# Kernel tuning notes

Measured on AMD Instinct MI355X. Metric: run time of the kernel, lower is better.

## Reference

```python
import jax, jax.numpy as jnp
import numpy as np

B, N = 32, 262144

def setup_inputs() -> dict:
    key = jax.random.key(0)
    k1, k2, k3, k4, k5 = jax.random.split(key, 5)
    F_mat = jax.random.normal(k1, (B, 3, 3), jnp.float32)
    f = 800.0 + 50.0 * jax.random.normal(k2, (B,), jnp.float32)
    K = (jnp.zeros((B, 3, 3), jnp.float32)
         .at[:, 0, 0].set(f).at[:, 1, 1].set(f)
         .at[:, 0, 2].set(320.0).at[:, 1, 2].set(240.0)
         .at[:, 2, 2].set(1.0))
    pts1_flat = jax.random.uniform(k3, (N, 2), jnp.float32) * 640.0
    pts2_flat = jax.random.uniform(k4, (N, 2), jnp.float32) * 640.0
    batch_indices = jnp.sort(jax.random.randint(k5, (N,), 0, B))
    return {"F_mat": F_mat, "K": K, "pts1_flat": pts1_flat,
            "pts2_flat": pts2_flat, "batch_indices": batch_indices}

def _pose_candidates(E):
    # torch.svd returns V (not V^T); the original code uses R = U @ W @ V.
    U, S, Vh = jnp.linalg.svd(E)
    U = U * jnp.where(jnp.linalg.det(U) < 0, -1.0, 1.0)[:, None, None]
    Vh = Vh * jnp.where(jnp.linalg.det(Vh) < 0, -1.0, 1.0)[:, None, None]
    V = jnp.swapaxes(Vh, -1, -2)  # = torch's "Vt" variable (which is V)
    W = jnp.array([[0.0, -1.0, 0.0], [1.0, 0.0, 0.0], [0.0, 0.0, 1.0]], E.dtype)
    R1 = U @ W @ V
    R2 = U @ W.T @ V
    t = U[:, :, 2]
    R_cand = jnp.stack([R1, R1, R2, R2], axis=1)          # [B,4,3,3]
    t_cand = jnp.stack([t, -t, t, -t], axis=1)            # [B,4,3]
    return R_cand, t_cand

def _cheirality_scores(R_cand, t_cand, K, pts1_flat, pts2_flat, batch_indices):
    n = pts1_flat.shape[0]
    Kinv = jnp.linalg.inv(K)[batch_indices]               # [N,3,3]
    ones = jnp.ones((n, 1), pts1_flat.dtype)
    p1 = jnp.einsum('nij,nj->ni', Kinv, jnp.concatenate([pts1_flat, ones], 1))[:, :2]
    p2 = jnp.einsum('nij,nj->ni', Kinv, jnp.concatenate([pts2_flat, ones], 1))[:, :2]
    P2 = jnp.concatenate([R_cand, t_cand[..., None]], axis=-1)  # [B,4,3,4]
    P2n = P2[batch_indices]                                     # [N,4,3,4]
    # A rows for P1 = [I|0]: A0 = [-1,0,x1,0], A1 = [0,-1,y1,0]
    z = jnp.zeros((n,), p1.dtype)
    A0 = jnp.stack([-jnp.ones_like(z), z, p1[:, 0], z], axis=-1)  # [N,4]
    A1 = jnp.stack([z, -jnp.ones_like(z), p1[:, 1], z], axis=-1)
    A2 = p2[:, 0, None, None] * P2n[:, :, 2, :] - P2n[:, :, 0, :]  # [N,4,4]
    A3 = p2[:, 1, None, None] * P2n[:, :, 2, :] - P2n[:, :, 1, :]
    A = jnp.stack([jnp.broadcast_to(A0[:, None, :], A2.shape),
                   jnp.broadcast_to(A1[:, None, :], A2.shape), A2, A3], axis=2)  # [N,4,4,4]
    _, _, Vh = jnp.linalg.svd(A)
    vec = Vh[..., :, -1]                      # = last ROW of V, faithful to torch code
    pts3d = vec[..., :3] / vec[..., 3:4]      # [N,4,3]
    z1 = pts3d[..., 2]                        # depth in cam 1 (P1 = [I|0])
    z2 = jnp.sum(P2n[:, :, 2, :3] * pts3d, axis=-1) + P2n[:, :, 2, 3]
    in_front = ((z1 > 0) & (z2 > 0)).astype(jnp.float32)  # [N,4]
    scores = jax.ops.segment_sum(in_front, batch_indices, num_segments=B)  # [B,4]
    counts = jax.ops.segment_sum(jnp.ones((n,), jnp.float32), batch_indices, num_segments=B)
    return scores, counts

def reference(F_mat, K, pts1_flat, pts2_flat, batch_indices):
    E = jnp.einsum('bji,bjk,bkl->bil', K, F_mat, K)       # K^T F K
    R_cand, t_cand = _pose_candidates(E)
    scores, counts = _cheirality_scores(R_cand, t_cand, K, pts1_flat, pts2_flat, batch_indices)
    best_idx = jnp.argmax(scores, axis=1)                 # first max, like torch '>'
    has = (counts > 0).astype(R_cand.dtype)
    bi = jnp.arange(B)
    best_R = R_cand[bi, best_idx] * has[:, None, None]
    best_t = t_cand[bi, best_idx] * has[:, None]
    best_candidate = jnp.where(counts > 0, best_idx, 0)
    return best_R, best_t, best_candidate
```

## Files before the change

### kernel.cpp

```cpp
#include <hip/hip_runtime.h>
#include <math.h>


#define NBATCH 32
#define USE_NEW_SLARTG 1

#define EPS4  5.9604645e-08f
#define UNFL4 1.1754944e-38f
#define TOL4  (10.0f * EPS4)


__device__ __forceinline__ float sign_f(float a, float b) {
  return (b >= 0.0f) ? fabsf(a) : -fabsf(a);
}

__device__ __forceinline__ float slapy2f(float x, float y) {
#pragma clang fp contract(off)
  float xa = fabsf(x), ya = fabsf(y);
  float w = fmaxf(xa, ya), z = fminf(xa, ya);
  if (z == 0.0f) return w;
  float r = z / w;
  return w * sqrtf(1.0f + r * r);
}

// ... 89 lines not shown
      float mm_ = gt / ft;
      float t = 2.0f - l;
      float mm = mm_ * mm_, tt = t * t;
      float s = sqrtf(tt + mm);
      float r;
      if (l == 0.0f) r = fabsf(mm_); else r = sqrtf(l * l + mm);
      float a = 0.5f * (s + r);
      *ssmin = ha / a;
      *ssmax = fa * a;
      if (mm == 0.0f) {
        if (l == 0.0f) t = sign_f(2.0f, ft) * sign_f(1.0f, gt);
        else t = gt / sign_f(dd, ft) + mm_ / t;
      } else {
        t = (mm_ / (s + t) + mm_ / (r + l)) * (1.0f + a);
      }
      float l2 = sqrtf(t * t + 4.0f);
      crt = 2.0f / l2;
      srt = t / l2;
      clt = (crt + srt * mm_) / a;
      slt = (ht / ft) * srt / a;
    }
  }
  if (swap_) { *csl = srt; *snl = crt; *csr = slt; *snr = clt; }
  else { *csl = clt; *snl = slt; *csr = crt; *snr = srt; }
  float tsign = 1.0f;
  if (pmax == 1) tsign = sign_f(1.0f, *csr) * sign_f(1.0f, *csl) * sign_f(1.0f, f);
  if (pmax == 2) tsign = sign_f(1.0f, *snr) * sign_f(1.0f, *csl) * sign_f(1.0f, g);
  if (pmax == 3) tsign = sign_f(1.0f, *snr) * sign_f(1.0f, *snl) * sign_f(1.0f, h);
  *ssmax = sign_f(*ssmax, tsign);
  *ssmin = sign_f(*ssmin, tsign * sign_f(1.0f, f) * sign_f(1.0f, h));
}


template <int NN, bool WANTU>
__device__ void sbdsqr_t(float* d, float* e, float VT[4][4], float U[4][4]) {
#pragma clang fp contract(off)
  const int n = NN;
  const float EPS = EPS4;
  const float UNFL = UNFL4;
  const float TOL = TOL4;
  const int MAXITR = 6;

  float sminoa = fabsf(d[0]);
  if (sminoa != 0.0f) {
    float mu = sminoa;
    for (int i = 2; i <= n; i++) {
      mu = fabsf(d[i - 1]) * (mu / (mu + fabsf(e[i - 2])));
      if (mu < sminoa) sminoa = mu;
      if (sminoa == 0.0f) break;
    }
  }
  sminoa = sminoa / sqrtf((float)n);
  float thresh = fmaxf(TOL * sminoa, (float)(MAXITR * n * n) * UNFL);

  int maxit = MAXITR * n * n;
  int iter = 0, oldll = -1, oldm = -1, idir = 0;
  int m = n;
  float sminl = 0.0f;
  int guard = 0;

  while (guard++ < 1000) {
    if (m <= 1) break;
    if (iter > maxit) break;

    float smax = fabsf(d[m - 1]);
    float smin = smax; (void)smin;
    int ll = 0;
    bool split = false;
    for (int lll = 1; lll <= m - 1; lll++) {
      ll = m - lll;
      float abss = fabsf(d[ll - 1]);
      float abse = fabsf(e[ll - 1]);
      if (abse <= thresh) { split = true; break; }
      if (abss < smin) smin = abss;
      float mx = fmaxf(abss, abse);
      if (mx > smax) smax = mx;
    }
    if (split) {
      e[ll - 1] = 0.0f;
      if (ll == m - 1) { m = m - 1; continue; }
      ll = ll + 1;
    } else {
      ll = 1;
    }
    if (ll == m - 1) {
      float sigmn, sigmx, sinr, cosr, sinl, cosl;
      slasv2_(d[m - 2], e[m - 2], d[m - 1], &sigmn, &sigmx, &sinr, &cosr, &sinl, &cosl);
      d[m - 2] = sigmx; e[m - 2] = 0.0f; d[m - 1] = sigmn;
      for (int k = 0; k < n; k++) {
        float x = VT[m - 2][k], y = VT[m - 1][k];
        VT[m - 2][k] = cosr * x + sinr * y; VT[m - 1][k] = cosr * y - sinr * x;
      }
      if (WANTU) {
        for (int k = 0; k < n; k++) {
          float x = U[k][m - 2], y = U[k][m - 1];
          U[k][m - 2] = cosl * x + sinl * y; U[k][m - 1] = cosl * y - sinl * x;
        }
      }
      m -= 2;
      continue;
    }
    if (ll > oldm || m < oldll)
      idir = (fabsf(d[ll - 1]) >= fabsf(d[m - 1])) ? 1 : 2;

    bool deflated = false;
    if (idir == 1) {
      if (fabsf(e[m - 2]) <= TOL * fabsf(d[m - 1])) { e[m - 2] = 0.0f; continue; }
      float mu = fabsf(d[ll - 1]); sminl = mu;
      for (int lll = ll; lll <= m - 1; lll++) {
        if (fabsf(e[lll - 1]) <= TOL * mu) { e[lll - 1] = 0.0f; deflated = true; break; }
        mu = fabsf(d[lll]) * (mu / (mu + fabsf(e[lll - 1])));
        if (mu < sminl) sminl = mu;
      }
    } else {
      if (fabsf(e[ll - 1]) <= TOL * fabsf(d[ll - 1])) { e[ll - 1] = 0.0f; continue; }
      float mu = fabsf(d[m - 1]); sminl = mu;
      for (int lll = m - 1; lll >= ll; lll--) {
        if (fabsf(e[lll - 1]) <= TOL * mu) { e[lll - 1] = 0.0f; deflated = true; break; }
        mu = fabsf(d[lll - 1]) * (mu / (mu + fabsf(e[lll - 1])));
        if (mu < sminl) sminl = mu;
      }
    }
    if (deflated) continue;
    oldll = ll; oldm = m;

    float shift = 0.0f, rdum;
    if (!((float)n * TOL * (sminl / smax) <= fmaxf(EPS, 0.01f * TOL))) {
      float sll;
      if (idir == 1) { sll = fabsf(d[ll - 1]); slas2_(d[m - 2], e[m - 2], d[m - 1], &shift, &rdum); }
      else { sll = fabsf(d[m - 1]); slas2_(d[ll - 1], e[ll - 1], d[ll], &shift, &rdum); }
      if (sll > 0.0f) {
        float q = shift / sll;
        if (q * q < EPS) shift = 0.0f;
      }
    }
    iter += m - ll;

    if (shift == 0.0f) {
      if (idir == 1) {
        float cs = 1.0f, oldcs = 1.0f, sn = 0.0f, oldsn = 0.0f, r = 0.0f;
        for (int i = ll; i <= m - 1; i++) {
          float c1, s1;
          slartg_(d[i - 1] * cs, e[i - 1], &c1, &s1, &r);
          cs = c1; sn = s1;
          if (i > ll) e[i - 2] = oldsn * r;
          float c2, s2, rr;
          slartg_(oldcs * r, d[i] * sn, &c2, &s2, &rr);
          oldcs = c2; oldsn = s2;
          d[i - 1] = rr;
          for (int k = 0; k < n; k++) {
            float x = VT[i - 1][k], y = VT[i][k];
            VT[i - 1][k] = cs * x + sn * y; VT[i][k] = cs * y - sn * x;
          }
          if (WANTU) {
            for (int k = 0; k < n; k++) {
              float x = U[k][i - 1], y = U[k][i];
              U[k][i - 1] = oldcs * x + oldsn * y; U[k][i] = oldcs * y - oldsn * x;
            }
          }
        }
        float h = d[m - 1] * cs;
        d[m - 1] = h * oldcs;
        e[m - 2] = h * oldsn;
        if (fabsf(e[m - 2]) <= thresh) e[m - 2] = 0.0f;
      } else {
        float cs = 1.0f, oldcs = 1.0f, sn = 0.0f, oldsn = 0.0f, r = 0.0f;
        for (int i = m; i >= ll + 1; i--) {
          float c1, s1;
          slartg_(d[i - 1] * cs, e[i - 2], &c1, &s1, &r);
          cs = c1; sn = s1;
          if (i < m) e[i - 1] = oldsn * r;
          float c2, s2, rr;
          slartg_(oldcs * r, d[i - 2] * sn, &c2, &s2, &rr);
          oldcs = c2; oldsn = s2;
          d[i - 1] = rr;
          if (WANTU) {
            for (int k = 0; k < n; k++) {
              float x = U[k][i - 1], y = U[k][i - 2];
              U[k][i - 1] = cs * x + sn * y; U[k][i - 2] = cs * y - sn * x;
            }
          }
          for (int k = 0; k < n; k++) {
            float x = VT[i - 1][k], y = VT[i - 2][k];
            VT[i - 1][k] = oldcs * x + oldsn * y; VT[i - 2][k] = oldcs * y - oldsn * x;
          }
        }
        float h = d[ll - 1] * cs;
        d[ll - 1] = h * oldcs;
        e[ll - 1] = h * oldsn;
        if (fabsf(e[ll - 1]) <= thresh) e[ll - 1] = 0.0f;
      }
    } else {
      if (idir == 1) {
        float f = (fabsf(d[ll - 1]) - shift) * (sign_f(1.0f, d[ll - 1]) + shift / d[ll - 1]);
        float g = e[ll - 1];
        for (int i = ll; i <= m - 1; i++) {
          float cosr, sinr, r;
          slartg_(f, g, &cosr, &sinr, &r);
          if (i > ll) e[i - 2] = r;
          f = cosr * d[i - 1] + sinr * e[i - 1];
          e[i - 1] = cosr * e[i - 1] - sinr * d[i - 1];
          g = sinr * d[i];
          d[i] = cosr * d[i];
          float cosl, sinl, rr;
          slartg_(f, g, &cosl, &sinl, &rr);
          d[i - 1] = rr;
          f = cosl * e[i - 1] + sinl * d[i];
          d[i] = cosl * d[i] - sinl * e[i - 1];
          if (i < m - 1) {
            g = sinl * e[i];
            e[i] = cosl * e[i];
          }
          for (int k = 0; k < n; k++) {
            float x = VT[i - 1][k], y = VT[i][k];
            VT[i - 1][k] = cosr * x + sinr * y; VT[i][k] = cosr * y - sinr * x;
          }
          if (WANTU) {
            for (int k = 0; k < n; k++) {
              float x = U[k][i - 1], y = U[k][i];
              U[k][i - 1] = cosl * x + sinl * y; U[k][i] = cosl * y - sinl * x;
            }
          }
        }
        e[m - 2] = f;
        if (fabsf(e[m - 2]) <= thresh) e[m - 2] = 0.0f;
      } else {
        float f = (fabsf(d[m - 1]) - shift) * (sign_f(1.0f, d[m - 1]) + shift / d[m - 1]);
        float g = e[m - 2];
        for (int i = m; i >= ll + 1; i--) {
          float cosr, sinr, r;
          slartg_(f, g, &cosr, &sinr, &r);
          if (i < m) e[i - 1] = r;
          f = cosr * d[i - 1] + sinr * e[i - 2];
          e[i - 2] = cosr * e[i - 2] - sinr * d[i - 1];
          g = sinr * d[i - 2];
          d[i - 2] = cosr * d[i - 2];
          float cosl, sinl, rr;
          slartg_(f, g, &cosl, &sinl, &rr);
          d[i - 1] = rr;
          f = cosl * e[i - 2] + sinl * d[i - 2];
          d[i - 2] = cosl * d[i - 2] - sinl * e[i - 2];
          if (i > ll + 1) {
            g = sinl * e[i - 3];
            e[i - 3] = cosl * e[i - 3];
          }
          if (WANTU) {
            for (int k = 0; k < n; k++) {
              float x = U[k][i - 1], y = U[k][i - 2];
              U[k][i - 1] = cosr * x + sinr * y; U[k][i - 2] = cosr * y - sinr * x;
            }
          }
          for (int k = 0; k < n; k++) {
            float x = VT[i - 1][k], y = VT[i - 2][k];
            VT[i - 1][k] = cosl * x + sinl * y; VT[i - 2][k] = cosl * y - sinl * x;
          }
        }
        e[ll - 1] = f;
        if (fabsf(e[ll - 1]) <= thresh) e[ll - 1] = 0.0f;
      }
    }
  }

  for (int i = 0; i < n; i++) {
    if (d[i] < 0.0f) {
      d[i] = -d[i];
      for (int k = 0; k < n; k++) VT[i][k] = -VT[i][k];
    }
  }
  for (int i = 1; i <= n - 1; i++) {
    int isub = 1; float smn = d[0];
    for (int j = 2; j <= n + 1 - i; j++) {
      if (d[j - 1] <= smn) { isub = j; smn = d[j - 1]; }
    }
    if (isub != n + 1 - i) {
      d[isub - 1] = d[n - i]; d[n - i] = smn;
      for (int k = 0; k < n; k++) { float t = VT[isub - 1][k]; VT[isub - 1][k] = VT[n - i][k]; VT[n - i][k] = t; }
      if (WANTU) {
        for (int k = 0; k < n; k++) { float t = U[k][isub - 1]; U[k][isub - 1] = U[k][n - i]; U[k][n - i] = t; }
      }
    }
  }
}

template <int NN, bool WANTU>
__device__ void gesdd_small(const float* A0, float U[4][4], float VT[4][4]) {
#pragma clang fp contract(off)
  const int n = NN;
  float a[4][4];
  for (int i = 0; i < n; i++) for (int j = 0; j < n; j++) a[i][j] = A0[i * n + j];
  float d[4], e[4], tauq[4], taup[4];

  for (int i = 0; i < n; i++) {
    float alpha = a[i][i];
    float ss = 0.0f;
    for (int r = i + 1; r < n; r++) ss += a[r][i] * a[r][i];
    if (ss == 0.0f) { tauq[i] = 0.0f; d[i] = alpha; }
    else {
      float xnorm = sqrtf(ss);
      float beta = -sign_f(slapy2f(alpha, xnorm), alpha);
      tauq[i] = (beta - alpha) / beta;
      float scal = 1.0f / (alpha - beta);
      for (int r = i + 1; r < n; r++) a[r][i] *= scal;
      d[i] = beta;
    }
    for (int c = i + 1; c < n; c++) {
      float w = a[i][c];
      for (int r = i + 1; r < n; r++) w += a[r][i] * a[r][c];
      float tw = tauq[i] * w;
      a[i][c] -= tw;
      for (int r = i + 1; r < n; r++) a[r][c] -= tw * a[r][i];
    }
    if (i < n - 1) {
      float alpha2 = a[i][i + 1];
      float ss2 = 0.0f;
      for (int c = i + 2; c < n; c++) ss2 += a[i][c] * a[i][c];
      if (ss2 == 0.0f) { taup[i] = 0.0f; e[i] = alpha2; }
      else {
        float xnorm = sqrtf(ss2);
        float beta = -sign_f(slapy2f(alpha2, xnorm), alpha2);
        taup[i] = (beta - alpha2) / beta;
        float scal = 1.0f / (alpha2 - beta);
        for (int c = i + 2; c < n; c++) a[i][c] *= scal;
        e[i] = beta;
      }
      for (int r = i + 1; r < n; r++) {
        float w = a[r][i + 1];
        for (int c = i + 2; c < n; c++) w += a[r][c] * a[i][c];
        float tw = taup[i] * w;
        a[r][i + 1] -= tw;
        for (int c = i + 2; c < n; c++) a[r][c] -= tw * a[i][c];
      }
    }
  }

  for (int i = 0; i < n; i++) for (int j = 0; j < n; j++) {
    VT[i][j] = (i == j) ? 1.0f : 0.0f;
    if (WANTU) U[i][j] = (i == j) ? 1.0f : 0.0f;
  }
  sbdsqr_t<NN, WANTU>(d, e, VT, U);

  if (WANTU) {
    for (int i = n - 1; i >= 0; i--) {
      for (int c = 0; c < n; c++) {
        float w = U[i][c];
        for (int r = i + 1; r < n; r++) w += a[r][i] * U[r][c];
        float tw = tauq[i] * w;
        U[i][c] -= tw;
        for (int r = i + 1; r < n; r++) U[r][c] -= tw * a[r][i];
      }
    }
  }
  for (int i = n - 2; i >= 0; i--) {
    for (int r = 0; r < n; r++) {
      float w = VT[r][i + 1];
      for (int c = i + 2; c < n; c++) w += VT[r][c] * a[i][c];
      float tw = taup[i] * w;
      VT[r][i + 1] -= tw;
      for (int c = i + 2; c < n; c++) VT[r][c] -= tw * a[i][c];
    }
  }
}

__device__ __forceinline__ float det3f(const float M[4][4]) {
#pragma clang fp contract(off)
  return M[0][0] * (M[1][1] * M[2][2] - M[1][2] * M[2][1])
       - M[0][1] * (M[1][0] * M[2][2] - M[1][2] * M[2][0])
       + M[0][2] * (M[1][0] * M[2][1] - M[1][1] * M[2][0]);
}


template <int LL, int M>
__device__ __forceinline__ void sv_chase(float (&d)[4], float (&e)[3], float (&vt)[4][4],
                                         float thresh, int& iter, int& oldll, int& oldm,
                                         int& idir, float smax) {
#pragma clang fp contract(off)
  if (LL > oldm || M < oldll)
    idir = (fabsf(d[LL - 1]) >= fabsf(d[M - 1])) ? 1 : 2;

  bool deflated = false;
  float sminl = 0.0f;
  if (idir == 1) {
    if (fabsf(e[M - 2]) <= TOL4 * fabsf(d[M - 1])) { e[M - 2] = 0.0f; return; }
    float mu = fabsf(d[LL - 1]); sminl = mu;
#pragma unroll
    for (int lll = LL; lll <= M - 1; lll++) {
      if (!deflated) {
        if (fabsf(e[lll - 1]) <= TOL4 * mu) { e[lll - 1] = 0.0f; deflated = true; }
        else {
          mu = fabsf(d[lll]) * (mu / (mu + fabsf(e[lll - 1])));
          if (mu < sminl) sminl = mu;
        }
      }
    }
  } else {
    if (fabsf(e[LL - 1]) <= TOL4 * fabsf(d[LL - 1])) { e[LL - 1] = 0.0f; return; }
    float mu = fabsf(d[M - 1]); sminl = mu;
// ... 361 lines not shown
    vt[r][1] -= tw;
    vt[r][2] -= tw * a[0][2];
    vt[r][3] -= tw * a[0][3];
  }

  vec[0] = vt[0][3]; vec[1] = vt[1][3]; vec[2] = vt[2][3]; vec[3] = vt[3][3];
}


__global__ __launch_bounds__(64) void pose_kernel(const float* __restrict__ Fm,
                                                  const float* __restrict__ Km,
                                                  float* __restrict__ ws) {
  int b = blockIdx.x;
  if (threadIdx.x != 0 || b >= NBATCH) return;
  float* wsR = ws;
  float* wsT = ws + 1152;
  float* wsK = ws + 1536;
  int* scores = (int*)(ws + 1664);
  int* counts = (int*)(ws + 1792);
  for (int c = 0; c < 4; c++) scores[b * 4 + c] = 0;
  counts[b] = 0;
  {
#pragma clang fp contract(off)
    const float* F = Fm + b * 9;
    const float* K = Km + b * 9;
    float E[9];
    for (int i = 0; i < 3; i++) for (int l = 0; l < 3; l++) {
      float acc = 0.0f;
      for (int j = 0; j < 3; j++)
        for (int k = 0; k < 3; k++)
          acc += (K[j * 3 + i] * F[j * 3 + k]) * K[k * 3 + l];
      E[i * 3 + l] = acc;
    }
    float U[4][4], VT[4][4];
    gesdd_small<3, true>(E, U, VT);
    float su = (det3f(U) < 0.0f) ? -1.0f : 1.0f;
    float sv = (det3f(VT) < 0.0f) ? -1.0f : 1.0f;
    for (int i = 0; i < 3; i++) for (int j = 0; j < 3; j++) { U[i][j] *= su; VT[i][j] *= sv; }
    float R1[3][3], R2[3][3];
    for (int r = 0; r < 3; r++) {
      float uw0 = U[r][1], uw1 = -U[r][0], uw2 = U[r][2];
      float vw0 = -U[r][1], vw1 = U[r][0];
      for (int c = 0; c < 3; c++) {
        R1[r][c] = (uw0 * VT[c][0] + uw1 * VT[c][1]) + uw2 * VT[c][2];
        R2[r][c] = (vw0 * VT[c][0] + vw1 * VT[c][1]) + uw2 * VT[c][2];
      }
    }
    float t0 = U[0][2], t1 = U[1][2], t2 = U[2][2];
    for (int c = 0; c < 4; c++) {
      const float (*R)[3] = (c < 2) ? R1 : R2;
      float sg = (c & 1) ? -1.0f : 1.0f;
      float* dst = wsR + (b * 4 + c) * 9;
      for (int i = 0; i < 3; i++) for (int j = 0; j < 3; j++) dst[i * 3 + j] = R[i][j];
      float* dt = wsT + (b * 4 + c) * 3;
      dt[0] = sg * t0; dt[1] = sg * t1; dt[2] = sg * t2;
    }
    const float fx = K[0], fy = K[4], cx = K[2], cy = K[5];
    float invfx = 1.0f / fx, invfy = 1.0f / fy;
    wsK[b * 4 + 0] = invfx;
    wsK[b * 4 + 1] = -(invfx * cx);
    wsK[b * 4 + 2] = invfy;
    wsK[b * 4 + 3] = -(invfy * cy);
  }
}


__global__ __launch_bounds__(256) void score_kernel(const float* __restrict__ pts1,
                                                    const float* __restrict__ pts2,
                                                    const int* __restrict__ bidx,
                                                    float* __restrict__ ws,
                                                    int n_pts) {
  __shared__ float sR[1152];
  __shared__ float sT[384];
  __shared__ float sK[128];
  __shared__ int h01[32], h23[32], hc[32];
  int tid = threadIdx.x;
  for (int i = tid; i < 1152; i += 256) sR[i] = ws[i];
  for (int i = tid; i < 384; i += 256) sT[i] = ws[1152 + i];
  for (int i = tid; i < 128; i += 256) sK[i] = ws[1536 + i];
  if (tid < 32) { h01[tid] = 0; h23[tid] = 0; hc[tid] = 0; }
  __syncthreads();

  int gid = blockIdx.x * 256 + tid;
  int n = gid >> 1, pr = gid & 1;
  bool active = (n < n_pts);
  bool f0 = false, f1 = false;
  int b = 0;
  if (active) {
    b = bidx[n];
    float x1 = pts1[2 * n], y1 = pts1[2 * n + 1];
    float x2 = pts2[2 * n], y2 = pts2[2 * n + 1];
    float invfx = sK[b * 4 + 0], k02 = sK[b * 4 + 1];
    float invfy = sK[b * 4 + 2], k12 = sK[b * 4 + 3];
    const float* R = sR + (b * 4 + 2 * pr) * 9;
    const float* t = sT + (b * 4 + 2 * pr) * 3;
    float Am[16];
    float row2[4] = { R[6], R[7], R[8], t[2] };
    {
#pragma clang fp contract(off)
      float p1x = invfx * x1 + k02;
      float p1y = invfy * y1 + k12;
      float p2x = invfx * x2 + k02;
      float p2y = invfy * y2 + k12;
      float row0[4] = { R[0], R[1], R[2], t[0] };
      float row1[4] = { R[3], R[4], R[5], t[1] };
      Am[0] = -1.0f; Am[1] = 0.0f; Am[2] = p1x; Am[3] = 0.0f;
      Am[4] = 0.0f; Am[5] = -1.0f; Am[6] = p1y; Am[7] = 0.0f;
#pragma unroll
      for (int k = 0; k < 4; k++) {
        Am[8 + k] = p2x * row2[k] - row0[k];
        Am[12 + k] = p2y * row2[k] - row1[k];
      }
    }
    float vec[4];
    gesdd4_vec(Am, vec);
    {
#pragma clang fp contract(off)
      float v3 = vec[3];
      float X = vec[0] / v3, Y = vec[1] / v3, Z = vec[2] / v3;
      float p0 = row2[0] * X, p1 = row2[1] * Y, p2 = row2[2] * Z;
      float s = (p0 + p1) + p2;
      float t2 = row2[3];
      float z2a = s + t2;
      float z2b = s + (-t2);
      bool zpos = (Z > 0.0f);
      f0 = zpos && (z2a > 0.0f);
      f1 = zpos && (z2b > 0.0f);
    }
  }
  if (active) {
    int add = (f0 ? 1 : 0) | (f1 ? (1 << 16) : 0);
    if (add) {
      if (pr == 0) atomicAdd(&h01[b], add);
      else atomicAdd(&h23[b], add);
    }
    if (pr == 0) atomicAdd(&hc[b], 1);
  }
  __syncthreads();
  if (tid < 32) {
    int* scores = (int*)(ws + 1664);
    int* counts = (int*)(ws + 1792);
    int v01 = h01[tid], v23 = h23[tid], vc = hc[tid];
    if (v01 & 0xFFFF) atomicAdd(&scores[tid * 4 + 0], v01 & 0xFFFF);
    if (v01 >> 16) atomicAdd(&scores[tid * 4 + 1], v01 >> 16);
    if (v23 & 0xFFFF) atomicAdd(&scores[tid * 4 + 2], v23 & 0xFFFF);
    if (v23 >> 16) atomicAdd(&scores[tid * 4 + 3], v23 >> 16);
    if (vc) atomicAdd(&counts[tid], vc);
  }
}


__global__ __launch_bounds__(64) void final_kernel(const float* __restrict__ ws,
                                                   float* __restrict__ out) {
  int b = threadIdx.x;
  if (b >= NBATCH) return;
  const int* scores = (const int*)(ws + 1664);
  const int* counts = (const int*)(ws + 1792);
  int best = 0, bs = scores[b * 4];
  for (int c = 1; c < 4; c++) {
    int sc = scores[b * 4 + c];
    if (sc > bs) { bs = sc; best = c; }
  }
  int cnt = counts[b];
  float has = (cnt > 0) ? 1.0f : 0.0f;
  const float* R = ws + (b * 4 + best) * 9;
  const float* t = ws + 1152 + (b * 4 + best) * 3;
  for (int k = 0; k < 9; k++) out[b * 9 + k] = R[k] * has;
  for (int k = 0; k < 3; k++) out[288 + b * 3 + k] = t[k] * has;
  out[384 + b] = (cnt > 0) ? (float)best : 0.0f;
}


extern "C" void kernel_launch(void* const* d_in, const int* in_sizes, int n_in,
                              void* d_out, int out_size, void* d_ws, size_t ws_size,
                              hipStream_t stream) {
  (void)n_in; (void)out_size; (void)ws_size;
  const float* F = (const float*)d_in[0];
  const float* K = (const float*)d_in[1];
  const float* p1 = (const float*)d_in[2];
  const float* p2 = (const float*)d_in[3];
  const int* bi = (const int*)d_in[4];
  int n_pts = in_sizes[4];
  float* ws = (float*)d_ws;
  float* out = (float*)d_out;

  pose_kernel<<<NBATCH, 64, 0, stream>>>(F, K, ws);
  int total = n_pts * 2;
  int blocks = (total + 255) / 256;
  score_kernel<<<blocks, 256, 0, stream>>>(p1, p2, bi, ws, n_pts);
  final_kernel<<<1, 64, 0, stream>>>(ws, out);
}
```

Before: 219.8 us.

## Specialize pose SVD to 3x3, drop shared staging, use wave-ballot score reduction

Replaces the generic templated bidiagonal SVD in the pose kernel with a fully unrolled 3x3-specialized version. In the score kernel it removes shared-memory staging of R, t and K in favour of direct global reads, and halves the block size to 128. It also replaces the shared-memory histogram and per-block flush with wave-level ballot/popcount reductions that issue global atomics directly, falling back to per-thread atomics when a wave spans several batches. The aim is to cut per-block setup and barriers in the dominant score kernel. In exchange, more global atomics reach the same addresses.

```diff
diff --git a/kernel.cpp b/kernel.cpp
--- a/kernel.cpp
+++ b/kernel.cpp
@@ -145,336 +145,462 @@
 }
 
 
-template <int NN, bool WANTU>
-__device__ void sbdsqr_t(float* d, float* e, float VT[4][4], float U[4][4]) {
-#pragma clang fp contract(off)
-  const int n = NN;
-  const float EPS = EPS4;
-  const float UNFL = UNFL4;
-  const float TOL = TOL4;
-  const int MAXITR = 6;
-
-  float sminoa = fabsf(d[0]);
-  if (sminoa != 0.0f) {
-    float mu = sminoa;
-    for (int i = 2; i <= n; i++) {
-      mu = fabsf(d[i - 1]) * (mu / (mu + fabsf(e[i - 2])));
-      if (mu < sminoa) sminoa = mu;
-      if (sminoa == 0.0f) break;
-    }
-  }
-  sminoa = sminoa / sqrtf((float)n);
-  float thresh = fmaxf(TOL * sminoa, (float)(MAXITR * n * n) * UNFL);
-
-  int maxit = MAXITR * n * n;
-  int iter = 0, oldll = -1, oldm = -1, idir = 0;
-  int m = n;
+__device__ __forceinline__ void sv3_chase(float (&d)[3], float (&e)[2],
+                                          float (&vt)[3][3], float (&u)[3][3],
+                                          float thresh, int& iter, int& oldll,
+                                          int& oldm, int& idir, float smax) {
+#pragma clang fp contract(off)
+  if (1 > oldm || 3 < oldll)
+    idir = (fabsf(d[0]) >= fabsf(d[2])) ? 1 : 2;
+
+  bool deflated = false;
   float sminl = 0.0f;
-  int guard = 0;
-
-  while (guard++ < 1000) {
-    if (m <= 1) break;
-    if (iter > maxit) break;
-
-    float smax = fabsf(d[m - 1]);
-    float smin = smax; (void)smin;
-    int ll = 0;
-    bool split = false;
-    for (int lll = 1; lll <= m - 1; lll++) {
-      ll = m - lll;
-      float abss = fabsf(d[ll - 1]);
-      float abse = fabsf(e[ll - 1]);
-      if (abse <= thresh) { split = true; break; }
-      if (abss < smin) smin = abss;
-      float mx = fmaxf(abss, abse);
-      if (mx > smax) smax = mx;
-    }
-    if (split) {
-      e[ll - 1] = 0.0f;
-      if (ll == m - 1) { m = m - 1; continue; }
-      ll = ll + 1;
+  if (idir == 1) {
+    if (fabsf(e[1]) <= TOL4 * fabsf(d[2])) { e[1] = 0.0f; return; }
+    float mu = fabsf(d[0]); sminl = mu;
+    if (fabsf(e[0]) <= TOL4 * mu) { e[0] = 0.0f; deflated = true; }
+    else {
+      mu = fabsf(d[1]) * (mu / (mu + fabsf(e[0])));
+      if (mu < sminl) sminl = mu;
+      if (fabsf(e[1]) <= TOL4 * mu) { e[1] = 0.0f; deflated = true; }
+      else {
+        mu = fabsf(d[2]) * (mu / (mu + fabsf(e[1])));
+        if (mu < sminl) sminl = mu;
+      }
+    }
+  } else {
+    if (fabsf(e[0]) <= TOL4 * fabsf(d[0])) { e[0] = 0.0f; return; }
+    float mu = fabsf(d[2]); sminl = mu;
+    if (fabsf(e[1]) <= TOL4 * mu) { e[1] = 0.0f; deflated = true; }
+    else {
+      mu = fabsf(d[1]) * (mu / (mu + fabsf(e[1])));
+      if (mu < sminl) sminl = mu;
+      if (fabsf(e[0]) <= TOL4 * mu) { e[0] = 0.0f; deflated = true; }
+      else {
+        mu = fabsf(d[0]) * (mu / (mu + fabsf(e[0])));
+        if (mu < sminl) sminl = mu;
+      }
+    }
+  }
+  if (deflated) return;
+  oldll = 1; oldm = 3;
+
+  float shift = 0.0f, rdum;
+  if (!(3.0f * TOL4 * (sminl / smax) <= fmaxf(EPS4, 0.01f * TOL4))) {
+    float sll;
+    if (idir == 1) { sll = fabsf(d[0]); slas2_(d[1], e[1], d[2], &shift, &rdum); }
+    else { sll = fabsf(d[2]); slas2_(d[0], e[0], d[1], &shift, &rdum); }
+    if (sll > 0.0f) {
+      float q = shift / sll;
+      if (q * q < EPS4) shift = 0.0f;
+    }
+  }
+  iter += 2;
+
+  if (shift == 0.0f) {
+    if (idir == 1) {
+      float cs = 1.0f, oldcs = 1.0f, sn = 0.0f, oldsn = 0.0f, r = 0.0f;
+      float c1, s1, c2, s2, rr;
+      slartg_(d[0] * cs, e[0], &c1, &s1, &r); cs = c1; sn = s1;
+      slartg_(oldcs * r, d[1] * sn, &c2, &s2, &rr); oldcs = c2; oldsn = s2;
+      d[0] = rr;
+#pragma unroll
+      for (int k = 0; k < 3; k++) {
+        float x = vt[0][k], y = vt[1][k];
+        vt[0][k] = cs * x + sn * y; vt[1][k] = cs * y - sn * x;
+      }
+#pragma unroll
+      for (int k = 0; k < 3; k++) {
+        float x = u[k][0], y = u[k][1];
+        u[k][0] = oldcs * x + oldsn * y; u[k][1] = oldcs * y - oldsn * x;
+      }
+      slartg_(d[1] * cs, e[1], &c1, &s1, &r); cs = c1; sn = s1;
+      e[0] = oldsn * r;
+      slartg_(oldcs * r, d[2] * sn, &c2, &s2, &rr); oldcs = c2; oldsn = s2;
+      d[1] = rr;
+#pragma unroll
+      for (int k = 0; k < 3; k++) {
+        float x = vt[1][k], y = vt[2][k];
+        vt[1][k] = cs * x + sn * y; vt[2][k] = cs * y - sn * x;
+      }
+#pragma unroll
+      for (int k = 0; k < 3; k++) {
+        float x = u[k][1], y = u[k][2];
+        u[k][1] = oldcs * x + oldsn * y; u[k][2] = oldcs * y - oldsn * x;
+      }
+      float h = d[2] * cs;
+      d[2] = h * oldcs;
+      e[1] = h * oldsn;
+      if (fabsf(e[1]) <= thresh) e[1] = 0.0f;
     } else {
+      float cs = 1.0f, oldcs = 1.0f, sn = 0.0f, oldsn = 0.0f, r = 0.0f;
+      float c1, s1, c2, s2, rr;
+      slartg_(d[2] * cs, e[1], &c1, &s1, &r); cs = c1; sn = s1;
+      slartg_(oldcs * r, d[1] * sn, &c2, &s2, &rr); oldcs = c2; oldsn = s2;
+      d[2] = rr;
+#pragma unroll
+      for (int k = 0; k < 3; k++) {
+        float x = u[k][2], y = u[k][1];
+        u[k][2] = cs * x + sn * y; u[k][1] = cs * y - sn * x;
+      }
+#pragma unroll
+      for (int k = 0; k < 3; k++) {
+        float x = vt[2][k], y = vt[1][k];
+        vt[2][k] = oldcs * x + oldsn * y; vt[1][k] = oldcs * y - oldsn * x;
+      }
+      slartg_(d[1] * cs, e[0], &c1, &s1, &r); cs = c1; sn = s1;
+      e[1] = oldsn * r;
+      slartg_(oldcs * r, d[0] * sn, &c2, &s2, &rr); oldcs = c2; oldsn = s2;
+      d[1] = rr;
+#pragma unroll
+      for (int k = 0; k < 3; k++) {
+        float x = u[k][1], y = u[k][0];
+        u[k][1] = cs * x + sn * y; u[k][0] = cs * y - sn * x;
+      }
+#pragma unroll
+      for (int k = 0; k < 3; k++) {
+        float x = vt[1][k], y = vt[0][k];
+        vt[1][k] = oldcs * x + oldsn * y; vt[0][k] = oldcs * y - oldsn * x;
+      }
+      float h = d[0] * cs;
+      d[0] = h * oldcs;
+      e[0] = h * oldsn;
+      if (fabsf(e[0]) <= thresh) e[0] = 0.0f;
+    }
+  } else {
+    if (idir == 1) {
+      float f = (fabsf(d[0]) - shift) * (sign_f(1.0f, d[0]) + shift / d[0]);
+      float g = e[0];
+      float cosr, sinr, cosl, sinl, r, rr;
+      slartg_(f, g, &cosr, &sinr, &r);
+      f = cosr * d[0] + sinr * e[0];
+      e[0] = cosr * e[0] - sinr * d[0];
+      g = sinr * d[1];
+      d[1] = cosr * d[1];
+      slartg_(f, g, &cosl, &sinl, &rr);
+      d[0] = rr;
+      f = cosl * e[0] + sinl * d[1];
+      d[1] = cosl * d[1] - sinl * e[0];
+      g = sinl * e[1];
+      e[1] = cosl * e[1];
+#pragma unroll
+      for (int k = 0; k < 3; k++) {
+        float x = vt[0][k], y = vt[1][k];
+        vt[0][k] = cosr * x + sinr * y; vt[1][k] = cosr * y - sinr * x;
+      }
+#pragma unroll
+      for (int k = 0; k < 3; k++) {
+        float x = u[k][0], y = u[k][1];
+        u[k][0] = cosl * x + sinl * y; u[k][1] = cosl * y - sinl * x;
+      }
+      slartg_(f, g, &cosr, &sinr, &r);
+      e[0] = r;
+      f = cosr * d[1] + sinr * e[1];
+      e[1] = cosr * e[1] - sinr * d[1];
+      g = sinr * d[2];
+      d[2] = cosr * d[2];
+      slartg_(f, g, &cosl, &sinl, &rr);
+      d[1] = rr;
+      f = cosl * e[1] + sinl * d[2];
+      d[2] = cosl * d[2] - sinl * e[1];
+#pragma unroll
+      for (int k = 0; k < 3; k++) {
+        float x = vt[1][k], y = vt[2][k];
+        vt[1][k] = cosr * x + sinr * y; vt[2][k] = cosr * y - sinr * x;
+      }
+#pragma unroll
+      for (int k = 0; k < 3; k++) {
+        float x = u[k][1], y = u[k][2];
+        u[k][1] = cosl * x + sinl * y; u[k][2] = cosl * y - sinl * x;
+      }
+      e[1] = f;
+      if (fabsf(e[1]) <= thresh) e[1] = 0.0f;
+    } else {
+      float f = (fabsf(d[2]) - shift) * (sign_f(1.0f, d[2]) + shift / d[2]);
+      float g = e[1];
+      float cosr, sinr, cosl, sinl, r, rr;
+      slartg_(f, g, &cosr, &sinr, &r);
+      f = cosr * d[2] + sinr * e[1];
+      e[1] = cosr * e[1] - sinr * d[2];
+      g = sinr * d[1];
+      d[1] = cosr * d[1];
+      slartg_(f, g, &cosl, &sinl, &rr);
+      d[2] = rr;
+      f = cosl * e[1] + sinl * d[1];
+      d[1] = cosl * d[1] - sinl * e[1];
+      g = sinl * e[0];
+      e[0] = cosl * e[0];
+#pragma unroll
+      for (int k = 0; k < 3; k++) {
+        float x = u[k][2], y = u[k][1];
+        u[k][2] = cosr * x + sinr * y; u[k][1] = cosr * y - sinr * x;
+      }
+#pragma unroll
+      for (int k = 0; k < 3; k++) {
+        float x = vt[2][k], y = vt[1][k];
+        vt[2][k] = cosl * x + sinl * y; vt[1][k] = cosl * y - sinl * x;
+      }
+      slartg_(f, g, &cosr, &sinr, &r);
+      e[1] = r;
+      f = cosr * d[1] + sinr * e[0];
+      e[0] = cosr * e[0] - sinr * d[1];
+      g = sinr * d[0];
+      d[0] = cosr * d[0];
+      slartg_(f, g, &cosl, &sinl, &rr);
+      d[1] = rr;
+      f = cosl * e[0] + sinl * d[0];
+      d[0] = cosl * d[0] - sinl * e[0];
+#pragma unroll
+      for (int k = 0; k < 3; k++) {
+        float x = u[k][1], y = u[k][0];
+        u[k][1] = cosr * x + sinr * y; u[k][0] = cosr * y - sinr * x;
+      }
+#pragma unroll
+      for (int k = 0; k < 3; k++) {
+        float x = vt[1][k], y = vt[0][k];
+        vt[1][k] = cosl * x + sinl * y; vt[0][k] = cosl * y - sinl * x;
+      }
+      e[0] = f;
+      if (fabsf(e[0]) <= thresh) e[0] = 0.0f;
+    }
+  }
+}
+
+__device__ __forceinline__ void sv3_iter3(float (&d)[3], float (&e)[2],
+                                          float (&vt)[3][3], float (&u)[3][3],
+                                          float thresh, int& m, int& iter,
+                                          int& oldll, int& oldm, int& idir) {
+#pragma clang fp contract(off)
+  float smax = fabsf(d[2]);
+  int ll = 0;
+  bool split = false;
+  if (fabsf(e[1]) <= thresh) { split = true; ll = 2; }
+  else {
+    smax = fmaxf(smax, fmaxf(fabsf(d[1]), fabsf(e[1])));
+    if (fabsf(e[0]) <= thresh) { split = true; ll = 1; }
+    else {
+      smax = fmaxf(smax, fmaxf(fabsf(d[0]), fabsf(e[0])));
       ll = 1;
     }
-    if (ll == m - 1) {
-      float sigmn, sigmx, sinr, cosr, sinl, cosl;
-      slasv2_(d[m - 2], e[m - 2], d[m - 1], &sigmn, &sigmx, &sinr, &cosr, &sinl, &cosl);
-      d[m - 2] = sigmx; e[m - 2] = 0.0f; d[m - 1] = sigmn;
-      for (int k = 0; k < n; k++) {
-        float x = VT[m - 2][k], y = VT[m - 1][k];
-        VT[m - 2][k] = cosr * x + sinr * y; VT[m - 1][k] = cosr * y - sinr * x;
-      }
-      if (WANTU) {
-        for (int k = 0; k < n; k++) {
-          float x = U[k][m - 2], y = U[k][m - 1];
-          U[k][m - 2] = cosl * x + sinl * y; U[k][m - 1] = cosl * y - sinl * x;
-        }
-      }
-      m -= 2;
-      continue;
-    }
-    if (ll > oldm || m < oldll)
-      idir = (fabsf(d[ll - 1]) >= fabsf(d[m - 1])) ? 1 : 2;
-
-    bool deflated = false;
-    if (idir == 1) {
-      if (fabsf(e[m - 2]) <= TOL * fabsf(d[m - 1])) { e[m - 2] = 0.0f; continue; }
-      float mu = fabsf(d[ll - 1]); sminl = mu;
-      for (int lll = ll; lll <= m - 1; lll++) {
-        if (fabsf(e[lll - 1]) <= TOL * mu) { e[lll - 1] = 0.0f; deflated = true; break; }
-        mu = fabsf(d[lll]) * (mu / (mu + fabsf(e[lll - 1])));
-        if (mu < sminl) sminl = mu;
-      }
-    } else {
-      if (fabsf(e[ll - 1]) <= TOL * fabsf(d[ll - 1])) { e[ll - 1] = 0.0f; continue; }
-      float mu = fabsf(d[m - 1]); sminl = mu;
-      for (int lll = m - 1; lll >= ll; lll--) {
-        if (fabsf(e[lll - 1]) <= TOL * mu) { e[lll - 1] = 0.0f; deflated = true; break; }
-        mu = fabsf(d[lll - 1]) * (mu / (mu + fabsf(e[lll - 1])));
-        if (mu < sminl) sminl = mu;
-      }
-    }
-    if (deflated) continue;
-    oldll = ll; oldm = m;
-
-    float shift = 0.0f, rdum;
-    if (!((float)n * TOL * (sminl / smax) <= fmaxf(EPS, 0.01f * TOL))) {
-      float sll;
-      if (idir == 1) { sll = fabsf(d[ll - 1]); slas2_(d[m - 2], e[m - 2], d[m - 1], &shift, &rdum); }
-      else { sll = fabsf(d[m - 1]); slas2_(d[ll - 1], e[ll - 1], d[ll], &shift, &rdum); }
-      if (sll > 0.0f) {
-        float q = shift / sll;
-        if (q * q < EPS) shift = 0.0f;
-      }
-    }
-    iter += m - ll;
-
-    if (shift == 0.0f) {
-      if (idir == 1) {
-        float cs = 1.0f, oldcs = 1.0f, sn = 0.0f, oldsn = 0.0f, r = 0.0f;
-        for (int i = ll; i <= m - 1; i++) {
-          float c1, s1;
-          slartg_(d[i - 1] * cs, e[i - 1], &c1, &s1, &r);
-          cs = c1; sn = s1;
-          if (i > ll) e[i - 2] = oldsn * r;
-          float c2, s2, rr;
-          slartg_(oldcs * r, d[i] * sn, &c2, &s2, &rr);
-          oldcs = c2; oldsn = s2;
-          d[i - 1] = rr;
-          for (int k = 0; k < n; k++) {
-            float x = VT[i - 1][k], y = VT[i][k];
-            VT[i - 1][k] = cs * x + sn * y; VT[i][k] = cs * y - sn * x;
-          }
-          if (WANTU) {
-            for (int k = 0; k < n; k++) {
-              float x = U[k][i - 1], y = U[k][i];
-              U[k][i - 1] = oldcs * x + oldsn * y; U[k][i] = oldcs * y - oldsn * x;
-            }
-          }
-        }
-        float h = d[m - 1] * cs;
-        d[m - 1] = h * oldcs;
-        e[m - 2] = h * oldsn;
-        if (fabsf(e[m - 2]) <= thresh) e[m - 2] = 0.0f;
-      } else {
-        float cs = 1.0f, oldcs = 1.0f, sn = 0.0f, oldsn = 0.0f, r = 0.0f;
-        for (int i = m; i >= ll + 1; i--) {
-          float c1, s1;
-          slartg_(d[i - 1] * cs, e[i - 2], &c1, &s1, &r);
-          cs = c1; sn = s1;
-          if (i < m) e[i - 1] = oldsn * r;
-          float c2, s2, rr;
-          slartg_(oldcs * r, d[i - 2] * sn, &c2, &s2, &rr);
-          oldcs = c2; oldsn = s2;
-          d[i - 1] = rr;
-          if (WANTU) {
-            for (int k = 0; k < n; k++) {
-              float x = U[k][i - 1], y = U[k][i - 2];
-              U[k][i - 1] = cs * x + sn * y; U[k][i - 2] = cs * y - sn * x;
-            }
-          }
-          for (int k = 0; k < n; k++) {
-            float x = VT[i - 1][k], y = VT[i - 2][k];
-            VT[i - 1][k] = oldcs * x + oldsn * y; VT[i - 2][k] = oldcs * y - oldsn * x;
-          }
-        }
-        float h = d[ll - 1] * cs;
-        d[ll - 1] = h * oldcs;
-        e[ll - 1] = h * oldsn;
-        if (fabsf(e[ll - 1]) <= thresh) e[ll - 1] = 0.0f;
-      }
-    } else {
-      if (idir == 1) {
-        float f = (fabsf(d[ll - 1]) - shift) * (sign_f(1.0f, d[ll - 1]) + shift / d[ll - 1]);
-        float g = e[ll - 1];
-        for (int i = ll; i <= m - 1; i++) {
-          float cosr, sinr, r;
-          slartg_(f, g, &cosr, &sinr, &r);
-          if (i > ll) e[i - 2] = r;
-          f = cosr * d[i - 1] + sinr * e[i - 1];
-          e[i - 1] = cosr * e[i - 1] - sinr * d[i - 1];
-          g = sinr * d[i];
-          d[i] = cosr * d[i];
-          float cosl, sinl, rr;
-          slartg_(f, g, &cosl, &sinl, &rr);
-          d[i - 1] = rr;
-          f = cosl * e[i - 1] + sinl * d[i];
-          d[i] = cosl * d[i] - sinl * e[i - 1];
-          if (i < m - 1) {
-            g = sinl * e[i];
-            e[i] = cosl * e[i];
-          }
-          for (int k = 0; k < n; k++) {
-            float x = VT[i - 1][k], y = VT[i][k];
-            VT[i - 1][k] = cosr * x + sinr * y; VT[i][k] = cosr * y - sinr * x;
-          }
-          if (WANTU) {
-            for (int k = 0; k < n; k++) {
-              float x = U[k][i - 1], y = U[k][i];
-              U[k][i - 1] = cosl * x + sinl * y; U[k][i] = cosl * y - sinl * x;
-            }
-          }
-        }
-        e[m - 2] = f;
-        if (fabsf(e[m - 2]) <= thresh) e[m - 2] = 0.0f;
-      } else {
-        float f = (fabsf(d[m - 1]) - shift) * (sign_f(1.0f, d[m - 1]) + shift / d[m - 1]);
-        float g = e[m - 2];
-        for (int i = m; i >= ll + 1; i--) {
-          float cosr, sinr, r;
-          slartg_(f, g, &cosr, &sinr, &r);
-          if (i < m) e[i - 1] = r;
-          f = cosr * d[i - 1] + sinr * e[i - 2];
-          e[i - 2] = cosr * e[i - 2] - sinr * d[i - 1];
-          g = sinr * d[i - 2];
-          d[i - 2] = cosr * d[i - 2];
-          float cosl, sinl, rr;
-          slartg_(f, g, &cosl, &sinl, &rr);
-          d[i - 1] = rr;
-          f = cosl * e[i - 2] + sinl * d[i - 2];
-          d[i - 2] = cosl * d[i - 2] - sinl * e[i - 2];
-          if (i > ll + 1) {
-            g = sinl * e[i - 3];
-            e[i - 3] = cosl * e[i - 3];
-          }
-          if (WANTU) {
-            for (int k = 0; k < n; k++) {
-              float x = U[k][i - 1], y = U[k][i - 2];
-              U[k][i - 1] = cosr * x + sinr * y; U[k][i - 2] = cosr * y - sinr * x;
-            }
-          }
-          for (int k = 0; k < n; k++) {
-            float x = VT[i - 1][k], y = VT[i - 2][k];
-            VT[i - 1][k] = cosl * x + sinl * y; VT[i - 2][k] = cosl * y - sinl * x;
-          }
-        }
-        e[ll - 1] = f;
-        if (fabsf(e[ll - 1]) <= thresh) e[ll - 1] = 0.0f;
-      }
-    }
-  }
-
-  for (int i = 0; i < n; i++) {
-    if (d[i] < 0.0f) {
-      d[i] = -d[i];
-      for (int k = 0; k < n; k++) VT[i][k] = -VT[i][k];
-    }
-  }
-  for (int i = 1; i <= n - 1; i++) {
-    int isub = 1; float smn = d[0];
-    for (int j = 2; j <= n + 1 - i; j++) {
-      if (d[j - 1] <= smn) { isub = j; smn = d[j - 1]; }
-    }
-    if (isub != n + 1 - i) {
-      d[isub - 1] = d[n - i]; d[n - i] = smn;
-      for (int k = 0; k < n; k++) { float t = VT[isub - 1][k]; VT[isub - 1][k] = VT[n - i][k]; VT[n - i][k] = t; }
-      if (WANTU) {
-        for (int k = 0; k < n; k++) { float t = U[k][isub - 1]; U[k][isub - 1] = U[k][n - i]; U[k][n - i] = t; }
-      }
-    }
-  }
-}
-
-template <int NN, bool WANTU>
-__device__ void gesdd_small(const float* A0, float U[4][4], float VT[4][4]) {
-#pragma clang fp contract(off)
-  const int n = NN;
-  float a[4][4];
-  for (int i = 0; i < n; i++) for (int j = 0; j < n; j++) a[i][j] = A0[i * n + j];
-  float d[4], e[4], tauq[4], taup[4];
-
-  for (int i = 0; i < n; i++) {
-    float alpha = a[i][i];
-    float ss = 0.0f;
-    for (int r = i + 1; r < n; r++) ss += a[r][i] * a[r][i];
-    if (ss == 0.0f) { tauq[i] = 0.0f; d[i] = alpha; }
+  }
+  if (split) {
+    if (ll == 2) { e[1] = 0.0f; m = 2; return; }
+    e[0] = 0.0f;
+    float sigmn, sigmx, sinr, cosr, sinl, cosl;
+    slasv2_(d[1], e[1], d[2], &sigmn, &sigmx, &sinr, &cosr, &sinl, &cosl);
+    d[1] = sigmx; e[1] = 0.0f; d[2] = sigmn;
+#pragma unroll
+    for (int k = 0; k < 3; k++) {
+      float x = vt[1][k], y = vt[2][k];
+      vt[1][k] = cosr * x + sinr * y; vt[2][k] = cosr * y - sinr * x;
+    }
+#pragma unroll
+    for (int k = 0; k < 3; k++) {
+      float x = u[k][1], y = u[k][2];
+      u[k][1] = cosl * x + sinl * y; u[k][2] = cosl * y - sinl * x;
+    }
+    m = 1;
+    return;
+  }
+  sv3_chase(d, e, vt, u, thresh, iter, oldll, oldm, idir, smax);
+}
+
+__device__ __forceinline__ void sv3_iter2(float (&d)[3], float (&e)[2],
+                                          float (&vt)[3][3], float (&u)[3][3],
+                                          float thresh, int& m) {
+#pragma clang fp contract(off)
+  if (fabsf(e[0]) <= thresh) { e[0] = 0.0f; m = 1; return; }
+  float sigmn, sigmx, sinr, cosr, sinl, cosl;
+  slasv2_(d[0], e[0], d[1], &sigmn, &sigmx, &sinr, &cosr, &sinl, &cosl);
+  d[0] = sigmx; e[0] = 0.0f; d[1] = sigmn;
+#pragma unroll
+  for (int k = 0; k < 3; k++) {
+    float x = vt[0][k], y = vt[1][k];
+    vt[0][k] = cosr * x + sinr * y; vt[1][k] = cosr * y - sinr * x;
+  }
+#pragma unroll
+  for (int k = 0; k < 3; k++) {
+    float x = u[k][0], y = u[k][1];
+    u[k][0] = cosl * x + sinl * y; u[k][1] = cosl * y - sinl * x;
+  }
+  m = 0;
+}
+
+__device__ void gesdd3_pose(const float E[9], float (&u)[3][3], float (&vt)[3][3]) {
+#pragma clang fp contract(off)
+  float a[3][3];
+#pragma unroll
+  for (int i = 0; i < 3; i++)
+#pragma unroll
+    for (int j = 0; j < 3; j++) a[i][j] = E[i * 3 + j];
+  float d[3], e[2], tauq[3], taup[2];
+
+  {
+    float alpha = a[0][0];
+    float ss = a[1][0] * a[1][0] + a[2][0] * a[2][0];
+    if (ss == 0.0f) { tauq[0] = 0.0f; d[0] = alpha; }
     else {
       float xnorm = sqrtf(ss);
       float beta = -sign_f(slapy2f(alpha, xnorm), alpha);
-      tauq[i] = (beta - alpha) / beta;
+      tauq[0] = (beta - alpha) / beta;
       float scal = 1.0f / (alpha - beta);
-      for (int r = i + 1; r < n; r++) a[r][i] *= scal;
-      d[i] = beta;
-    }
-    for (int c = i + 1; c < n; c++) {
-      float w = a[i][c];
-      for (int r = i + 1; r < n; r++) w += a[r][i] * a[r][c];
-      float tw = tauq[i] * w;
-      a[i][c] -= tw;
-      for (int r = i + 1; r < n; r++) a[r][c] -= tw * a[r][i];
-    }
-    if (i < n - 1) {
-      float alpha2 = a[i][i + 1];
-      float ss2 = 0.0f;
-      for (int c = i + 2; c < n; c++) ss2 += a[i][c] * a[i][c];
-      if (ss2 == 0.0f) { taup[i] = 0.0f; e[i] = alpha2; }
-      else {
-        float xnorm = sqrtf(ss2);
-        float beta = -sign_f(slapy2f(alpha2, xnorm), alpha2);
-        taup[i] = (beta - alpha2) / beta;
-        float scal = 1.0f / (alpha2 - beta);
-        for (int c = i + 2; c < n; c++) a[i][c] *= scal;
-        e[i] = beta;
-      }
-      for (int r = i + 1; r < n; r++) {
-        float w = a[r][i + 1];
-        for (int c = i + 2; c < n; c++) w += a[r][c] * a[i][c];
-        float tw = taup[i] * w;
-        a[r][i + 1] -= tw;
-        for (int c = i + 2; c < n; c++) a[r][c] -= tw * a[i][c];
-      }
-    }
-  }
-
-  for (int i = 0; i < n; i++) for (int j = 0; j < n; j++) {
-    VT[i][j] = (i == j) ? 1.0f : 0.0f;
-    if (WANTU) U[i][j] = (i == j) ? 1.0f : 0.0f;
-  }
-  sbdsqr_t<NN, WANTU>(d, e, VT, U);
-
-  if (WANTU) {
-    for (int i = n - 1; i >= 0; i--) {
-      for (int c = 0; c < n; c++) {
-        float w = U[i][c];
-        for (int r = i + 1; r < n; r++) w += a[r][i] * U[r][c];
-        float tw = tauq[i] * w;
-        U[i][c] -= tw;
-        for (int r = i + 1; r < n; r++) U[r][c] -= tw * a[r][i];
-      }
-    }
-  }
-  for (int i = n - 2; i >= 0; i--) {
-    for (int r = 0; r < n; r++) {
-      float w = VT[r][i + 1];
-      for (int c = i + 2; c < n; c++) w += VT[r][c] * a[i][c];
-      float tw = taup[i] * w;
-      VT[r][i + 1] -= tw;
-      for (int c = i + 2; c < n; c++) VT[r][c] -= tw * a[i][c];
-    }
-  }
-}
-
-__device__ __forceinline__ float det3f(const float M[4][4]) {
+      a[1][0] *= scal; a[2][0] *= scal;
+      d[0] = beta;
+    }
+#pragma unroll
+    for (int c = 1; c < 3; c++) {
+      float w = (a[0][c] + a[1][0] * a[1][c]) + a[2][0] * a[2][c];
+      float tw = tauq[0] * w;
+      a[0][c] -= tw; a[1][c] -= tw * a[1][0]; a[2][c] -= tw * a[2][0];
+    }
+    float alpha2 = a[0][1];
+    float ss2 = a[0][2] * a[0][2];
+    if (ss2 == 0.0f) { taup[0] = 0.0f; e[0] = alpha2; }
+    else {
+      float xnorm = sqrtf(ss2);
+      float beta = -sign_f(slapy2f(alpha2, xnorm), alpha2);
+      taup[0] = (beta - alpha2) / beta;
+      float scal = 1.0f / (alpha2 - beta);
+      a[0][2] *= scal;
+      e[0] = beta;
+    }
+#pragma unroll
+    for (int r = 1; r < 3; r++) {
+      float w = a[r][1] + a[r][2] * a[0][2];
+      float tw = taup[0] * w;
+      a[r][1] -= tw; a[r][2] -= tw * a[0][2];
+    }
+  }
+  {
+    float alpha = a[1][1];
+    float ss = a[2][1] * a[2][1];
+    if (ss == 0.0f) { tauq[1] = 0.0f; d[1] = alpha; }
+    else {
+      float xnorm = sqrtf(ss);
+      float beta = -sign_f(slapy2f(alpha, xnorm), alpha);
+      tauq[1] = (beta - alpha) / beta;
+      float scal = 1.0f / (alpha - beta);
+      a[2][1] *= scal;
+      d[1] = beta;
+    }
+    {
+      float w = a[1][2] + a[2][1] * a[2][2];
+      float tw = tauq[1] * w;
+      a[1][2] -= tw; a[2][2] -= tw * a[2][1];
+    }
+    taup[1] = 0.0f; e[1] = a[1][2];
+    {
+      float w = a[2][2];
+      float tw = taup[1] * w;
+      a[2][2] -= tw;
+    }
+  }
+  tauq[2] = 0.0f;
+  d[2] = a[2][2];
+
+#pragma unroll
+  for (int i = 0; i < 3; i++)
+#pragma unroll
+    for (int j = 0; j < 3; j++) {
+      vt[i][j] = (i == j) ? 1.0f : 0.0f;
+      u[i][j] = (i == j) ? 1.0f : 0.0f;
+    }
+
+  {
+    float sminoa = fabsf(d[0]);
+    if (sminoa != 0.0f) {
+      float mu = sminoa;
+      mu = fabsf(d[1]) * (mu / (mu + fabsf(e[0])));
+      if (mu < sminoa) sminoa = mu;
+      if (sminoa != 0.0f) {
+        mu = fabsf(d[2]) * (mu / (mu + fabsf(e[1])));
+        if (mu < sminoa) sminoa = mu;
+      }
+    }
+    sminoa = sminoa / sqrtf(3.0f);
+    float thresh = fmaxf(TOL4 * sminoa, 54.0f * UNFL4);
+    int m = 3, iter = 0, oldll = -1, oldm = -1, idir = 0, guard = 0;
+    while (guard++ < 500) {
+      if (m <= 1 || iter > 54) break;
+      if (m == 3) sv3_iter3(d, e, vt, u, thresh, m, iter, oldll, oldm, idir);
+      else sv3_iter2(d, e, vt, u, thresh, m);
+    }
+  }
+
+#pragma unroll
+  for (int i = 0; i < 3; i++) {
+    if (d[i] < 0.0f) {
+      d[i] = -d[i];
+#pragma unroll
+      for (int k = 0; k < 3; k++) vt[i][k] = -vt[i][k];
+    }
+  }
+  {
+    int isub = 1; float smn = d[0];
+    if (d[1] <= smn) { isub = 2; smn = d[1]; }
+    if (d[2] <= smn) { isub = 3; smn = d[2]; }
+    if (isub != 3) {
+      if (isub == 1) {
+        d[0] = d[2];
+#pragma unroll
+        for (int k = 0; k < 3; k++) { float t = vt[0][k]; vt[0][k] = vt[2][k]; vt[2][k] = t; }
+#pragma unroll
+        for (int k = 0; k < 3; k++) { float t = u[k][0]; u[k][0] = u[k][2]; u[k][2] = t; }
+      } else {
+        d[1] = d[2];
+#pragma unroll
+        for (int k = 0; k < 3; k++) { float t = vt[1][k]; vt[1][k] = vt[2][k]; vt[2][k] = t; }
+#pragma unroll
+        for (int k = 0; k < 3; k++) { float t = u[k][1]; u[k][1] = u[k][2]; u[k][2] = t; }
+      }
+      d[2] = smn;
+    }
+  }
+  {
+    int isub = 1; float smn = d[0];
+    if (d[1] <= smn) { isub = 2; smn = d[1]; }
+    if (isub != 2) {
+      d[0] = d[1]; d[1] = smn;
+#pragma unroll
+      for (int k = 0; k < 3; k++) { float t = vt[0][k]; vt[0][k] = vt[1][k]; vt[1][k] = t; }
+#pragma unroll
+      for (int k = 0; k < 3; k++) { float t = u[k][0]; u[k][0] = u[k][1]; u[k][1] = t; }
+    }
+  }
+
+#pragma unroll
+  for (int c = 0; c < 3; c++) {
+    float w = u[2][c];
+    float tw = tauq[2] * w;
+    u[2][c] -= tw;
+  }
+#pragma unroll
+  for (int c = 0; c < 3; c++) {
+    float w = u[1][c] + a[2][1] * u[2][c];
+    float tw = tauq[1] * w;
+    u[1][c] -= tw; u[2][c] -= tw * a[2][1];
+  }
+#pragma unroll
+  for (int c = 0; c < 3; c++) {
+    float w = (u[0][c] + a[1][0] * u[1][c]) + a[2][0] * u[2][c];
+    float tw = tauq[0] * w;
+    u[0][c] -= tw; u[1][c] -= tw * a[1][0]; u[2][c] -= tw * a[2][0];
+  }
+#pragma unroll
+  for (int r = 0; r < 3; r++) {
+    float w = vt[r][2];
+    float tw = taup[1] * w;
+    vt[r][2] -= tw;
+  }
+#pragma unroll
+  for (int r = 0; r < 3; r++) {
+    float w = vt[r][1] + vt[r][2] * a[0][2];
+    float tw = taup[0] * w;
+    vt[r][1] -= tw; vt[r][2] -= tw * a[0][2];
+  }
+}
+
+__device__ __forceinline__ float det3f(const float M[3][3]) {
 #pragma clang fp contract(off)
   return M[0][0] * (M[1][1] * M[2][2] - M[1][2] * M[2][1])
        - M[0][1] * (M[1][0] * M[2][2] - M[1][2] * M[2][0])
@@ -902,8 +1028,8 @@
           acc += (K[j * 3 + i] * F[j * 3 + k]) * K[k * 3 + l];
       E[i * 3 + l] = acc;
     }
-    float U[4][4], VT[4][4];
-    gesdd_small<3, true>(E, U, VT);
+    float U[3][3], VT[3][3];
+    gesdd3_pose(E, U, VT);
     float su = (det3f(U) < 0.0f) ? -1.0f : 1.0f;
     float sv = (det3f(VT) < 0.0f) ? -1.0f : 1.0f;
     for (int i = 0; i < 3; i++) for (int j = 0; j < 3; j++) { U[i][j] *= su; VT[i][j] *= sv; }
@@ -935,23 +1061,13 @@
 }
 
 
-__global__ __launch_bounds__(256) void score_kernel(const float* __restrict__ pts1,
+__global__ __launch_bounds__(128) void score_kernel(const float* __restrict__ pts1,
                                                     const float* __restrict__ pts2,
                                                     const int* __restrict__ bidx,
                                                     float* __restrict__ ws,
                                                     int n_pts) {
-  __shared__ float sR[1152];
-  __shared__ float sT[384];
-  __shared__ float sK[128];
-  __shared__ int h01[32], h23[32], hc[32];
   int tid = threadIdx.x;
-  for (int i = tid; i < 1152; i += 256) sR[i] = ws[i];
-  for (int i = tid; i < 384; i += 256) sT[i] = ws[1152 + i];
-  for (int i = tid; i < 128; i += 256) sK[i] = ws[1536 + i];
-  if (tid < 32) { h01[tid] = 0; h23[tid] = 0; hc[tid] = 0; }
-  __syncthreads();
-
-  int gid = blockIdx.x * 256 + tid;
+  int gid = blockIdx.x * 128 + tid;
   int n = gid >> 1, pr = gid & 1;
   bool active = (n < n_pts);
   bool f0 = false, f1 = false;
@@ -960,10 +1076,11 @@
     b = bidx[n];
     float x1 = pts1[2 * n], y1 = pts1[2 * n + 1];
     float x2 = pts2[2 * n], y2 = pts2[2 * n + 1];
-    float invfx = sK[b * 4 + 0], k02 = sK[b * 4 + 1];
-    float invfy = sK[b * 4 + 2], k12 = sK[b * 4 + 3];
-    const float* R = sR + (b * 4 + 2 * pr) * 9;
-    const float* t = sT + (b * 4 + 2 * pr) * 3;
+    const float* kinv = ws + 1536 + b * 4;
+    float invfx = kinv[0], k02 = kinv[1];
+    float invfy = kinv[2], k12 = kinv[3];
+    const float* R = ws + (b * 4 + 2 * pr) * 9;
+    const float* t = ws + 1152 + (b * 4 + 2 * pr) * 3;
     float Am[16];
     float row2[4] = { R[6], R[7], R[8], t[2] };
     {
@@ -998,24 +1115,32 @@
       f1 = zpos && (z2b > 0.0f);
     }
   }
-  if (active) {
-    int add = (f0 ? 1 : 0) | (f1 ? (1 << 16) : 0);
-    if (add) {
-      if (pr == 0) atomicAdd(&h01[b], add);
-      else atomicAdd(&h23[b], add);
-    }
-    if (pr == 0) atomicAdd(&hc[b], 1);
-  }
-  __syncthreads();
-  if (tid < 32) {
-    int* scores = (int*)(ws + 1664);
-    int* counts = (int*)(ws + 1792);
-    int v01 = h01[tid], v23 = h23[tid], vc = hc[tid];
-    if (v01 & 0xFFFF) atomicAdd(&scores[tid * 4 + 0], v01 & 0xFFFF);
-    if (v01 >> 16) atomicAdd(&scores[tid * 4 + 1], v01 >> 16);
-    if (v23 & 0xFFFF) atomicAdd(&scores[tid * 4 + 2], v23 & 0xFFFF);
-    if (v23 >> 16) atomicAdd(&scores[tid * 4 + 3], v23 >> 16);
-    if (vc) atomicAdd(&counts[tid], vc);
+
+  int* scores = (int*)(ws + 1664);
+  int* counts = (int*)(ws + 1792);
+  int lane = tid & 63;
+  unsigned long long act_m = __ballot(active ? 1 : 0);
+  if (act_m != 0ULL) {
+    int b0 = __shfl(b, 0);
+    bool uni = __all((!active || (b == b0)) ? 1 : 0);
+    if (uni) {
+      unsigned long long mc = __ballot((active && pr == 0) ? 1 : 0);
+      unsigned long long m0 = __ballot((f0 && pr == 0) ? 1 : 0);
+      unsigned long long m1 = __ballot((f1 && pr == 0) ? 1 : 0);
+      unsigned long long m2 = __ballot((f0 && pr == 1) ? 1 : 0);
+      unsigned long long m3 = __ballot((f1 && pr == 1) ? 1 : 0);
+      if (lane == 0) {
+        if (mc) atomicAdd(&counts[b0], (int)__popcll(mc));
+        if (m0) atomicAdd(&scores[b0 * 4 + 0], (int)__popcll(m0));
+        if (m1) atomicAdd(&scores[b0 * 4 + 1], (int)__popcll(m1));
+        if (m2) atomicAdd(&scores[b0 * 4 + 2], (int)__popcll(m2));
+        if (m3) atomicAdd(&scores[b0 * 4 + 3], (int)__popcll(m3));
+      }
+    } else if (active) {
+      if (pr == 0) atomicAdd(&counts[b], 1);
+      if (f0) atomicAdd(&scores[b * 4 + 2 * pr], 1);
+      if (f1) atomicAdd(&scores[b * 4 + 2 * pr + 1], 1);
+    }
   }
 }
 
@@ -1056,7 +1181,7 @@
 
   pose_kernel<<<NBATCH, 64, 0, stream>>>(F, K, ws);
   int total = n_pts * 2;
-  int blocks = (total + 255) / 256;
-  score_kernel<<<blocks, 256, 0, stream>>>(p1, p2, bi, ws, n_pts);
+  int blocks = (total + 127) / 128;
+  score_kernel<<<blocks, 128, 0, stream>>>(p1, p2, bi, ws, n_pts);
   final_kernel<<<1, 64, 0, stream>>>(ws, out);
 }
```

Measured after the change: 249.4 us. +13.5%, slower.
